# Kernel optimization log

Measured on AMD Instinct MI355X. Metric: run time of the kernel, lower is better.

Reference implementation:

```python
import jax, jax.numpy as jnp
import numpy as np

NEG_SLOPE = 0.2
EPS = 1e-16


def gat_conv(x, edge_index, W, att_src, att_dst, bias, heads, out_ch, concat):
    """PyG-style GATConv (eval mode, add_self_loops=True)."""
    N = x.shape[0]
    h = (x @ W).reshape(N, heads, out_ch)              # [N,H,C]
    loop = jnp.arange(N, dtype=edge_index.dtype)
    src = jnp.concatenate([edge_index[0], loop])       # [E+N]
    dst = jnp.concatenate([edge_index[1], loop])
    a_src = jnp.sum(h * att_src, axis=-1)              # [N,H]
    a_dst = jnp.sum(h * att_dst, axis=-1)
    e = jax.nn.leaky_relu(a_src[src] + a_dst[dst], NEG_SLOPE)  # [E+N,H]
    # segment softmax over destination nodes
    m = jax.ops.segment_max(e, dst, num_segments=N)
    e = jnp.exp(e - m[dst])
    s = jax.ops.segment_sum(e, dst, num_segments=N)
    alpha = e / (s[dst] + EPS)                         # [E+N,H]
    msg = h[src] * alpha[..., None]                    # [E+N,H,C]
    out = jax.ops.segment_sum(msg, dst, num_segments=N)  # [N,H,C]
    out = out.reshape(N, heads * out_ch) if concat else out.mean(axis=1)
    return out + bias


def setup_inputs() -> dict:
    key = jax.random.key(0)
    ks = jax.random.split(key, 11)
    N, F, E = 100000, 128, 1600000
    H1, C1 = 4, 16
    H2, C2 = 1, 16
    return {
        "x": jax.random.normal(ks[0], (N, F), dtype=jnp.float32),
        "edge_index": jax.random.randint(ks[1], (2, E), 0, N, dtype=jnp.int64) if jax.config.jax_enable_x64 else jax.random.randint(ks[1], (2, E), 0, N).astype(jnp.int32),
        "W1": jax.random.normal(ks[2], (F, H1 * C1), dtype=jnp.float32) * 0.1,
        "att_src1": jax.random.normal(ks[3], (H1, C1), dtype=jnp.float32) * 0.1,
        "att_dst1": jax.random.normal(ks[4], (H1, C1), dtype=jnp.float32) * 0.1,
        "bias1": jax.random.normal(ks[5], (H1 * C1,), dtype=jnp.float32) * 0.1,
        "W2": jax.random.normal(ks[6], (H1 * C1, H2 * C2), dtype=jnp.float32) * 0.1,
        "att_src2": jax.random.normal(ks[7], (H2, C2), dtype=jnp.float32) * 0.1,
        "att_dst2": jax.random.normal(ks[8], (H2, C2), dtype=jnp.float32) * 0.1,
        "bias2": jax.random.normal(ks[9], (C2,), dtype=jnp.float32) * 0.1,
    }


def reference(x, edge_index, W1, att_src1, att_dst1, bias1, W2, att_src2, att_dst2, bias2):
    # dropout is identity in eval mode
    h = gat_conv(x, edge_index, W1, att_src1, att_dst1, bias1, heads=4, out_ch=16, concat=True)
    h = jax.nn.elu(h)
    h = gat_conv(h, edge_index, W2, att_src2, att_dst2, bias2, heads=1, out_ch=16, concat=False)
    return jax.nn.log_softmax(h, axis=1)
```

## Files before the change

### kernel.cpp

```cpp
#include <hip/hip_runtime.h>
#include <hip/hip_fp16.h>
#include <hip/hip_bf16.h>
#include <math.h>


#define LRELU(v) ((v) > 0.f ? (v) : 0.2f * (v))
#define BSH 8
#define BCAP 5120
#define CHK 8192

typedef __attribute__((ext_vector_type(8))) short short8;
typedef __attribute__((ext_vector_type(8))) _Float16 half8;
typedef __attribute__((ext_vector_type(4))) _Float16 half4;
typedef __attribute__((ext_vector_type(4))) float float4v;

static __device__ __forceinline__ short f2bf(float f) {
    __hip_bfloat16 b = __float2bfloat16(f);
    return *reinterpret_cast<short*>(&b);
}

__global__ __launch_bounds__(256) void k_scatter(const int* __restrict__ ei, int* __restrict__ cursor,
                                                 int* __restrict__ stage, int E, int NBK) {
    __shared__ int hist[512];
    __shared__ int cnt2[512];
    __shared__ int base[512];
    int tid = threadIdx.x;
    int e0 = blockIdx.x * CHK;
    int nedge = E - e0; if (nedge > CHK) nedge = CHK;

    for (int i = tid; i < 512; i += 256) { hist[i] = 0; cnt2[i] = 0; }
    __syncthreads();
    for (int j = tid; j < nedge; j += 256) {
        int d = ei[E + e0 + j];
        atomicAdd(&hist[d >> BSH], 1);
    }
    __syncthreads();
    for (int b = tid; b < NBK; b += 256) {
        int c = hist[b];
        if (c > 0) base[b] = b * BCAP + atomicAdd(&cursor[b], c);
    }
    __syncthreads();
    for (int j = tid; j < nedge; j += 256) {
        int s = ei[e0 + j];
        int d = ei[E + e0 + j];
        int b = d >> BSH;
        int r = atomicAdd(&cnt2[b], 1);
        stage[base[b] + r] = s | ((d & ((1 << BSH) - 1)) << 17);
    }
}

__global__ __launch_bounds__(256) void k_build(const int* __restrict__ stage,
                                               const int* __restrict__ cursor,
                                               int* __restrict__ row_start,
                                               int* __restrict__ csr,
                                               const float* __restrict__ W1,
                                               const float* __restrict__ att_src,
                                               const float* __restrict__ att_dst,
                                               float* __restrict__ Wc,
                                               const float* __restrict__ W2,
                                               const float* __restrict__ att_src2,
                                               const float* __restrict__ att_dst2,
                                               float* __restrict__ Wc2,
                                               int NBK, int E, int N) {
    __shared__ int cnt[256];
    __shared__ int lb[256];
    __shared__ int cur[256];
    __shared__ int sA[256];
    int b = blockIdx.x, tid = threadIdx.x;
    int nodes0 = b << BSH;
    int nnodes = N - nodes0; if (nnodes > 256) nnodes = 256;
    int partial = 0;
    for (int i = tid; i < b; i += 256) partial += cursor[i];
    sA[tid] = partial;
    __syncthreads();
    for (int off = 128; off >= 1; off >>= 1) {
        if (tid < off) sA[tid] += sA[tid + off];
        __syncthreads();
    }
    int ebase = sA[0];
    int ecnt = cursor[b];
    __syncthreads();
    if (b == 0) {
        if (tid == 0) row_start[N] = E + N;
        for (int i = tid; i < 16 * 128; i += 256) {
            int col = i >> 7, k = i & 127;
            float v = 0.f;
            if (col < 8) {
                int h = col & 3;
                const float* att = (col < 4) ? att_src : att_dst;
                #pragma unroll
                for (int c = 0; c < 16; c++) v += W1[k * 64 + h * 16 + c] * att[h * 16 + c];
            }
            Wc[i] = v;
        }
        for (int i = tid; i < 128; i += 256) {
            int col = i >> 6, k = i & 63;
            const float* att = col ? att_dst2 : att_src2;
            float v = 0.f;
            #pragma unroll
            for (int c = 0; c < 16; c++) v += W2[k * 16 + c] * att[c];
            Wc2[i] = v;
        }
    }
    const int* sbk = stage + b * BCAP;
    cnt[tid] = (tid < nnodes) ? 1 : 0;
    __syncthreads();
    for (int e = tid; e < ecnt; e += 256) {
        int l = (sbk[e] >> 17) & 255;
        atomicAdd(&cnt[l], 1);
    }
    __syncthreads();
    int myc = cnt[tid];
    sA[tid] = myc;
    __syncthreads();
    for (int off = 1; off < 256; off <<= 1) {
        int r = sA[tid] + ((tid >= off) ? sA[tid - off] : 0);
        __syncthreads();
        sA[tid] = r;
        __syncthreads();
    }
    int gb = ebase + nodes0;
    lb[tid] = sA[tid] - myc;
    cur[tid] = 1;
    __syncthreads();
    if (tid < nnodes) {
        row_start[nodes0 + tid] = gb + lb[tid];
        csr[gb + lb[tid]] = nodes0 + tid;
    }
    __syncthreads();
    for (int e = tid; e < ecnt; e += 256) {
        int v = sbk[e];
        int l = (v >> 17) & 255;
        int src = v & 0x1FFFF;
        int r = atomicAdd(&cur[l], 1);
        csr[gb + lb[l] + r] = src;
    }
}

__global__ __launch_bounds__(256) void k_gemm1(const float* __restrict__ x,
                                               const float* __restrict__ W1,
                                               const float* __restrict__ Wc,
                                               __half* __restrict__ h1, float* __restrict__ a_src,
                                               float* __restrict__ a_dst, int N) {
    __shared__ short wt[80 * 136];
    int tid = threadIdx.x;
    for (int i = tid; i < 128 * 64; i += 256) {
        int k = i >> 6, c = i & 63;
        wt[c * 136 + k] = f2bf(W1[i]);
    }
    for (int i = tid; i < 16 * 128; i += 256) {
        int col = i >> 7, k = i & 127;
        wt[(64 + col) * 136 + k] = f2bf(Wc[i]);
    }
    __syncthreads();
    int wave = tid >> 6, lane = tid & 63;
    int m = lane & 15, q = lane >> 4;
    int nbase = blockIdx.x * 64 + wave * 16;
    int anode = nbase + m;
    bool rowok = anode < N;
    const float* xrow = x + (size_t)(rowok ? anode : 0) * 128 + q * 8;

    float4v acc[5];
    #pragma unroll
    for (int ct = 0; ct < 5; ct++)
        #pragma unroll
        for (int r = 0; r < 4; r++) acc[ct][r] = 0.f;

    #pragma unroll
    for (int kc = 0; kc < 4; kc++) {
        float4 u0 = make_float4(0.f, 0.f, 0.f, 0.f), u1 = u0;
        if (rowok) {
            u0 = *(const float4*)(xrow + kc * 32);
            u1 = *(const float4*)(xrow + kc * 32 + 4);
        }
        short8 af;
        af[0] = f2bf(u0.x); af[1] = f2bf(u0.y); af[2] = f2bf(u0.z); af[3] = f2bf(u0.w);
        af[4] = f2bf(u1.x); af[5] = f2bf(u1.y); af[6] = f2bf(u1.z); af[7] = f2bf(u1.w);
        #pragma unroll
        for (int ct = 0; ct < 5; ct++) {
            short8 bf = *(const short8*)&wt[(ct * 16 + m) * 136 + kc * 32 + q * 8];
            acc[ct] = __builtin_amdgcn_mfma_f32_16x16x32_bf16(af, bf, acc[ct], 0, 0, 0);
        }
    }
    #pragma unroll
    for (int ct = 0; ct < 4; ct++) {
        #pragma unroll
        for (int r = 0; r < 4; r++) {
            int n = nbase + q * 4 + r;
            if (n < N) h1[(size_t)n * 64 + ct * 16 + m] = __float2half(acc[ct][r]);
        }
    }
    #pragma unroll
    for (int r = 0; r < 4; r++) {
        int n = nbase + q * 4 + r;
        if (n < N) {
            float v = acc[4][r];
            if (m < 4) a_src[n * 4 + m] = v;
            else if (m < 8) a_dst[n * 4 + (m - 4)] = v;
        }
    }
}

__global__ __launch_bounds__(256) void k_agg1(const int* __restrict__ row_start,
                                              const int* __restrict__ csr_src,
                                              const float* __restrict__ a_src,
                                              const float* __restrict__ a_dst,
                                              const __half* __restrict__ h1,
                                              const float* __restrict__ bias,
                                              __half* __restrict__ out1, int N) {
    int tid = threadIdx.x;
    int wave = tid >> 6, lane = tid & 63;
    int grp = lane >> 2, sub = lane & 3;
    int node = blockIdx.x * 64 + wave * 16 + grp;
    if (node >= N) return;
    int row = row_start[node];
    int deg = row_start[node + 1] - row;
    float adm = a_dst[node * 4 + sub];
    const _Float16* hb = (const _Float16*)h1 + sub * 16;
    float A[16];
    #pragma unroll
    for (int c = 0; c < 16; c++) A[c] = 0.f;
    float sh = 0.f;
    int j = 0;
    for (; j + 4 <= deg; j += 4) {
        int s0 = csr_src[row + j + 0];
        int s1 = csr_src[row + j + 1];
        int s2 = csr_src[row + j + 2];
        int s3 = csr_src[row + j + 3];
        float x0 = a_src[s0 * 4 + sub] + adm;
        float x1 = a_src[s1 * 4 + sub] + adm;
        float x2 = a_src[s2 * 4 + sub] + adm;
        float x3 = a_src[s3 * 4 + sub] + adm;
        half8 p0 = *(const half8*)(hb + (size_t)s0 * 64);
        half8 q0 = *(const half8*)(hb + (size_t)s0 * 64 + 8);
        half8 p1 = *(const half8*)(hb + (size_t)s1 * 64);
        half8 q1 = *(const half8*)(hb + (size_t)s1 * 64 + 8);
        half8 p2 = *(const half8*)(hb + (size_t)s2 * 64);
        half8 q2 = *(const half8*)(hb + (size_t)s2 * 64 + 8);
        half8 p3 = *(const half8*)(hb + (size_t)s3 * 64);
        half8 q3 = *(const half8*)(hb + (size_t)s3 * 64 + 8);
        float e0 = __expf(fmaxf(x0, 0.2f * x0));
        float e1 = __expf(fmaxf(x1, 0.2f * x1));
        float e2 = __expf(fmaxf(x2, 0.2f * x2));
        float e3 = __expf(fmaxf(x3, 0.2f * x3));
        sh += (e0 + e1) + (e2 + e3);
        #pragma unroll
        for (int c = 0; c < 8; c++) {
            A[c]     += e0 * (float)p0[c] + e1 * (float)p1[c]
                      + e2 * (float)p2[c] + e3 * (float)p3[c];
            A[c + 8] += e0 * (float)q0[c] + e1 * (float)q1[c]
                      + e2 * (float)q2[c] + e3 * (float)q3[c];
        }
    }
    for (; j < deg; j++) {
        int s = csr_src[row + j];
        float xv = a_src[s * 4 + sub] + adm;
        half8 p = *(const half8*)(hb + (size_t)s * 64);
        half8 q = *(const half8*)(hb + (size_t)s * 64 + 8);
        float e = __expf(fmaxf(xv, 0.2f * xv));
        sh += e;
        #pragma unroll
        for (int c = 0; c < 8; c++) {
            A[c]     += e * (float)p[c];
            A[c + 8] += e * (float)q[c];
        }
    }
    float iv = 1.f / (sh + 1e-16f);
    const float4* bb = (const float4*)bias + sub * 4;
    union { __half2 h2v[8]; float4 f4[2]; } pk;
    #pragma unroll
    for (int c4 = 0; c4 < 4; c4++) {
        float4 b = bb[c4];
        float o0 = A[c4 * 4 + 0] * iv + b.x;
        float o1 = A[c4 * 4 + 1] * iv + b.y;
        float o2 = A[c4 * 4 + 2] * iv + b.z;
        float o3 = A[c4 * 4 + 3] * iv + b.w;
        o0 = (o0 > 0.f) ? o0 : (__expf(o0) - 1.f);
        o1 = (o1 > 0.f) ? o1 : (__expf(o1) - 1.f);
        o2 = (o2 > 0.f) ? o2 : (__expf(o2) - 1.f);
        o3 = (o3 > 0.f) ? o3 : (__expf(o3) - 1.f);
        pk.h2v[c4 * 2 + 0] = __floats2half2_rn(o0, o1);
        pk.h2v[c4 * 2 + 1] = __floats2half2_rn(o2, o3);
    }
    *(float4*)&out1[(size_t)node * 64 + sub * 16]     = pk.f4[0];
    *(float4*)&out1[(size_t)node * 64 + sub * 16 + 8] = pk.f4[1];
}

__global__ __launch_bounds__(256) void k_gemm2(const __half* __restrict__ out1,
                                               const float* __restrict__ W2,
                                               const float* __restrict__ Wc2,
                                               __half* __restrict__ h2, float* __restrict__ a_src,
                                               float* __restrict__ a_dst, int N) {
    __shared__ _Float16 wt2[16][72];
    __shared__ _Float16 wtb[16][72];
    int tid = threadIdx.x;
    for (int i = tid; i < 16 * 64; i += 256) {
        int k = i >> 4, c = i & 15;
        wt2[c][k] = (_Float16)W2[i];
    }
    for (int i = tid; i < 16 * 64; i += 256) {
        int col = i >> 6, k = i & 63;
        wtb[col][k] = (col < 2) ? (_Float16)Wc2[col * 64 + k] : (_Float16)0.f;
    }
    __syncthreads();
    int wave = tid >> 6, lane = tid & 63;
    int m = lane & 15, q = lane >> 4;
    int nbase = blockIdx.x * 64 + wave * 16;
    int anode = nbase + m;
    bool ok = anode < N;
    const __half* arow = out1 + (size_t)(ok ? anode : 0) * 64 + q * 8;

    float4v c1 = {0.f, 0.f, 0.f, 0.f}, c2v = {0.f, 0.f, 0.f, 0.f};
    #pragma unroll
    for (int kc = 0; kc < 2; kc++) {
        half8 af = *(const half8*)(arow + kc * 32);
        half8 b1 = *(const half8*)&wt2[m][kc * 32 + q * 8];
        half8 b2 = *(const half8*)&wtb[m][kc * 32 + q * 8];
        c1  = __builtin_amdgcn_mfma_f32_16x16x32_f16(af, b1, c1, 0, 0, 0);
        c2v = __builtin_amdgcn_mfma_f32_16x16x32_f16(af, b2, c2v, 0, 0, 0);
    }
    #pragma unroll
    for (int r = 0; r < 4; r++) {
        int n = nbase + q * 4 + r;
        if (n < N) {
            h2[(size_t)n * 16 + m] = __float2half(c1[r]);
            if (m == 0) a_src[n] = c2v[r];
            else if (m == 1) a_dst[n] = c2v[r];
        }
    }
}

__global__ __launch_bounds__(256) void k_agg2(const int* __restrict__ row_start,
                                              const int* __restrict__ csr_src,
                                              const float* __restrict__ a_src,
                                              const float* __restrict__ a_dst,
                                              const __half* __restrict__ h2,
                                              const float* __restrict__ bias,
                                              float* __restrict__ out, int N) {
    int tid = threadIdx.x;
    int wave = tid >> 6, lane = tid & 63;
    int grp = lane >> 2, sub = lane & 3;
    int node = blockIdx.x * 64 + wave * 16 + grp;
    if (node >= N) return;
    int row = row_start[node];
    int deg = row_start[node + 1] - row;
    float ad = a_dst[node];
    const _Float16* hb = (const _Float16*)h2 + sub * 4;
    float A0 = 0.f, A1 = 0.f, A2 = 0.f, A3 = 0.f;
    float sh = 0.f;
    int j = 0;
    for (; j + 4 <= deg; j += 4) {
        int s0 = csr_src[row + j + 0];
        int s1 = csr_src[row + j + 1];
        int s2 = csr_src[row + j + 2];
        int s3 = csr_src[row + j + 3];
        float x0 = a_src[s0] + ad;
        float x1 = a_src[s1] + ad;
        float x2 = a_src[s2] + ad;
        float x3 = a_src[s3] + ad;
        half4 v0 = *(const half4*)(hb + (size_t)s0 * 16);
        half4 v1 = *(const half4*)(hb + (size_t)s1 * 16);
        half4 v2 = *(const half4*)(hb + (size_t)s2 * 16);
        half4 v3 = *(const half4*)(hb + (size_t)s3 * 16);
        float e0 = __expf(fmaxf(x0, 0.2f * x0));
        float e1 = __expf(fmaxf(x1, 0.2f * x1));
        float e2 = __expf(fmaxf(x2, 0.2f * x2));
        float e3 = __expf(fmaxf(x3, 0.2f * x3));
        sh += (e0 + e1) + (e2 + e3);
        A0 += e0 * (float)v0[0] + e1 * (float)v1[0] + e2 * (float)v2[0] + e3 * (float)v3[0];
        A1 += e0 * (float)v0[1] + e1 * (float)v1[1] + e2 * (float)v2[1] + e3 * (float)v3[1];
        A2 += e0 * (float)v0[2] + e1 * (float)v1[2] + e2 * (float)v2[2] + e3 * (float)v3[2];
        A3 += e0 * (float)v0[3] + e1 * (float)v1[3] + e2 * (float)v2[3] + e3 * (float)v3[3];
    }
    for (; j < deg; j++) {
        int s = csr_src[row + j];
        float xv = a_src[s] + ad;
        half4 v = *(const half4*)(hb + (size_t)s * 16);
        float e = __expf(fmaxf(xv, 0.2f * xv));
        sh += e;
        A0 += e * (float)v[0];
        A1 += e * (float)v[1];
        A2 += e * (float)v[2];
        A3 += e * (float)v[3];
    }
    float iv = 1.f / (sh + 1e-16f);
    float4 b = ((const float4*)bias)[sub];
    float v0 = A0 * iv + b.x;
    float v1 = A1 * iv + b.y;
    float v2 = A2 * iv + b.z;
    float v3 = A3 * iv + b.w;
    float mx = fmaxf(fmaxf(v0, v1), fmaxf(v2, v3));
    mx = fmaxf(mx, __shfl_xor(mx, 1, 64));
    mx = fmaxf(mx, __shfl_xor(mx, 2, 64));
    float se = __expf(v0 - mx) + __expf(v1 - mx) + __expf(v2 - mx) + __expf(v3 - mx);
    se += __shfl_xor(se, 1, 64);
    se += __shfl_xor(se, 2, 64);
    float ls = mx + __logf(se);
    *(float4*)&out[(size_t)node * 16 + sub * 4] =
        make_float4(v0 - ls, v1 - ls, v2 - ls, v3 - ls);
}

extern "C" void kernel_launch(void* const* d_in, const int* in_sizes, int n_in,
                              void* d_out, int out_size, void* d_ws, size_t ws_size,
                              hipStream_t stream) {
    const float* x        = (const float*)d_in[0];
    const int*   ei       = (const int*)d_in[1];
    const float* W1       = (const float*)d_in[2];
    const float* att_src1 = (const float*)d_in[3];
    const float* att_dst1 = (const float*)d_in[4];
    const float* bias1    = (const float*)d_in[5];
    const float* W2       = (const float*)d_in[6];
    const float* att_src2 = (const float*)d_in[7];
    const float* att_dst2 = (const float*)d_in[8];
    const float* bias2    = (const float*)d_in[9];
    float* out = (float*)d_out;

    const int N = in_sizes[0] / 128;
    const int E = in_sizes[1] / 2;
    const int NBK = (N + 255) >> BSH;

    char* p = (char*)d_ws;
    auto alloc = [&](size_t bytes) -> void* {
        void* r = (void*)p;
        p += (bytes + 255) & ~(size_t)255;
        return r;
    };
    __half* h1     = (__half*)alloc((size_t)N * 64 * 2);
    __half* out1   = (__half*)alloc((size_t)N * 64 * 2);
    __half* h2     = (__half*)alloc((size_t)N * 16 * 2);
    float* a_src1  = (float*)alloc((size_t)N * 4 * 4);
    float* a_dst1  = (float*)alloc((size_t)N * 4 * 4);
    float* a_src2  = (float*)alloc((size_t)N * 4);
    float* a_dst2  = (float*)alloc((size_t)N * 4);
    float* Wc      = (float*)alloc(16 * 128 * 4);
    float* Wc2     = (float*)alloc(2 * 64 * 4);
    int*   row_st  = (int*)alloc((size_t)(N + 1) * 4);
    int*   csr     = (int*)alloc((size_t)(E + N) * 4);
    int*   stage   = (int*)alloc((size_t)NBK * BCAP * 4);
    int*   cursor  = (int*)alloc((size_t)NBK * 4);
    (void)ws_size; (void)n_in; (void)out_size;

    hipMemsetAsync(cursor, 0, (size_t)NBK * 4, stream);
    k_scatter<<<(E + CHK - 1) / CHK, 256, 0, stream>>>(ei, cursor, stage, E, NBK);
    k_build<<<NBK, 256, 0, stream>>>(stage, cursor, row_st, csr,
                                     W1, att_src1, att_dst1, Wc,
                                     W2, att_src2, att_dst2, Wc2, NBK, E, N);
    k_gemm1<<<(N + 63) / 64, 256, 0, stream>>>(x, W1, Wc, h1, a_src1, a_dst1, N);
    k_agg1<<<(N + 63) / 64, 256, 0, stream>>>(row_st, csr, a_src1, a_dst1, h1, bias1, out1, N);
    k_gemm2<<<(N + 63) / 64, 256, 0, stream>>>(out1, W2, Wc2, h2, a_src2, a_dst2, N);
    k_agg2<<<(N + 63) / 64, 256, 0, stream>>>(row_st, csr, a_src2, a_dst2, h2, bias2, out, N);
}
```

Measured before the change: 236.6 us.

## Split each node's edges across two lane groups and prefetch CSR indices

Both aggregation kernels now give each destination node 8 lanes instead of 4. The two 4-lane halves handle alternating edges, and their partial sums are combined with an xor-shuffle before the epilogue. The next batch of source indices is loaded one iteration ahead so the dependent gathers can issue sooner. This doubles thread-level parallelism on the gather-bound loops, which average about 17 edges per node. The cost is twice as many blocks, extra shuffle reductions, and idle lanes in the epilogue.

```diff
diff --git a/kernel.cpp b/kernel.cpp
--- a/kernel.cpp
+++ b/kernel.cpp
@@ -210,23 +210,23 @@
                                               __half* __restrict__ out1, int N) {
     int tid = threadIdx.x;
     int wave = tid >> 6, lane = tid & 63;
-    int grp = lane >> 2, sub = lane & 3;
-    int node = blockIdx.x * 64 + wave * 16 + grp;
+    int grp = lane >> 3, sub = lane & 3, par = (lane >> 2) & 1;
+    int node = blockIdx.x * 32 + wave * 8 + grp;
     if (node >= N) return;
     int row = row_start[node];
     int deg = row_start[node + 1] - row;
     float adm = a_dst[node * 4 + sub];
     const _Float16* hb = (const _Float16*)h1 + sub * 16;
+    const int* cp = csr_src + row + par;
     float A[16];
     #pragma unroll
     for (int c = 0; c < 16; c++) A[c] = 0.f;
     float sh = 0.f;
+    int c0 = 0, c1 = 0, c2 = 0, c3 = 0;
+    if (deg >= 8) { c0 = cp[0]; c1 = cp[2]; c2 = cp[4]; c3 = cp[6]; }
     int j = 0;
-    for (; j + 4 <= deg; j += 4) {
-        int s0 = csr_src[row + j + 0];
-        int s1 = csr_src[row + j + 1];
-        int s2 = csr_src[row + j + 2];
-        int s3 = csr_src[row + j + 3];
+    for (; j + 8 <= deg; j += 8) {
+        int s0 = c0, s1 = c1, s2 = c2, s3 = c3;
         float x0 = a_src[s0 * 4 + sub] + adm;
         float x1 = a_src[s1 * 4 + sub] + adm;
         float x2 = a_src[s2 * 4 + sub] + adm;
@@ -239,6 +239,9 @@
         half8 q2 = *(const half8*)(hb + (size_t)s2 * 64 + 8);
         half8 p3 = *(const half8*)(hb + (size_t)s3 * 64);
         half8 q3 = *(const half8*)(hb + (size_t)s3 * 64 + 8);
+        if (j + 16 <= deg) {
+            c0 = cp[j + 8]; c1 = cp[j + 10]; c2 = cp[j + 12]; c3 = cp[j + 14];
+        }
         float e0 = __expf(fmaxf(x0, 0.2f * x0));
         float e1 = __expf(fmaxf(x1, 0.2f * x1));
         float e2 = __expf(fmaxf(x2, 0.2f * x2));
@@ -252,38 +255,46 @@
                       + e2 * (float)q2[c] + e3 * (float)q3[c];
         }
     }
-    for (; j < deg; j++) {
-        int s = csr_src[row + j];
-        float xv = a_src[s * 4 + sub] + adm;
-        half8 p = *(const half8*)(hb + (size_t)s * 64);
-        half8 q = *(const half8*)(hb + (size_t)s * 64 + 8);
-        float e = __expf(fmaxf(xv, 0.2f * xv));
-        sh += e;
+    for (; j < deg; j += 2) {
+        int idx = j + par;
+        if (idx < deg) {
+            int s = csr_src[row + idx];
+            float xv = a_src[s * 4 + sub] + adm;
+            half8 p = *(const half8*)(hb + (size_t)s * 64);
+            half8 q = *(const half8*)(hb + (size_t)s * 64 + 8);
+            float e = __expf(fmaxf(xv, 0.2f * xv));
+            sh += e;
+            #pragma unroll
+            for (int c = 0; c < 8; c++) {
+                A[c]     += e * (float)p[c];
+                A[c + 8] += e * (float)q[c];
+            }
+        }
+    }
+    sh += __shfl_xor(sh, 4, 64);
+    #pragma unroll
+    for (int c = 0; c < 16; c++) A[c] += __shfl_xor(A[c], 4, 64);
+    if (par == 0) {
+        float iv = 1.f / (sh + 1e-16f);
+        const float4* bb = (const float4*)bias + sub * 4;
+        union { __half2 h2v[8]; float4 f4[2]; } pk;
         #pragma unroll
-        for (int c = 0; c < 8; c++) {
-            A[c]     += e * (float)p[c];
-            A[c + 8] += e * (float)q[c];
-        }
-    }
-    float iv = 1.f / (sh + 1e-16f);
-    const float4* bb = (const float4*)bias + sub * 4;
-    union { __half2 h2v[8]; float4 f4[2]; } pk;
-    #pragma unroll
-    for (int c4 = 0; c4 < 4; c4++) {
-        float4 b = bb[c4];
-        float o0 = A[c4 * 4 + 0] * iv + b.x;
-        float o1 = A[c4 * 4 + 1] * iv + b.y;
-        float o2 = A[c4 * 4 + 2] * iv + b.z;
-        float o3 = A[c4 * 4 + 3] * iv + b.w;
-        o0 = (o0 > 0.f) ? o0 : (__expf(o0) - 1.f);
-        o1 = (o1 > 0.f) ? o1 : (__expf(o1) - 1.f);
-        o2 = (o2 > 0.f) ? o2 : (__expf(o2) - 1.f);
-        o3 = (o3 > 0.f) ? o3 : (__expf(o3) - 1.f);
-        pk.h2v[c4 * 2 + 0] = __floats2half2_rn(o0, o1);
-        pk.h2v[c4 * 2 + 1] = __floats2half2_rn(o2, o3);
-    }
-    *(float4*)&out1[(size_t)node * 64 + sub * 16]     = pk.f4[0];
-    *(float4*)&out1[(size_t)node * 64 + sub * 16 + 8] = pk.f4[1];
+        for (int c4 = 0; c4 < 4; c4++) {
+            float4 b = bb[c4];
+            float o0 = A[c4 * 4 + 0] * iv + b.x;
+            float o1 = A[c4 * 4 + 1] * iv + b.y;
+            float o2 = A[c4 * 4 + 2] * iv + b.z;
+            float o3 = A[c4 * 4 + 3] * iv + b.w;
+            o0 = (o0 > 0.f) ? o0 : (__expf(o0) - 1.f);
+            o1 = (o1 > 0.f) ? o1 : (__expf(o1) - 1.f);
+            o2 = (o2 > 0.f) ? o2 : (__expf(o2) - 1.f);
+            o3 = (o3 > 0.f) ? o3 : (__expf(o3) - 1.f);
+            pk.h2v[c4 * 2 + 0] = __floats2half2_rn(o0, o1);
+            pk.h2v[c4 * 2 + 1] = __floats2half2_rn(o2, o3);
+        }
+        *(float4*)&out1[(size_t)node * 64 + sub * 16]     = pk.f4[0];
+        *(float4*)&out1[(size_t)node * 64 + sub * 16 + 8] = pk.f4[1];
+    }
 }
 
 __global__ __launch_bounds__(256) void k_gemm2(const __half* __restrict__ out1,
@@ -339,21 +350,21 @@
                                               float* __restrict__ out, int N) {
     int tid = threadIdx.x;
     int wave = tid >> 6, lane = tid & 63;
-    int grp = lane >> 2, sub = lane & 3;
-    int node = blockIdx.x * 64 + wave * 16 + grp;
+    int grp = lane >> 3, sub = lane & 3, par = (lane >> 2) & 1;
+    int node = blockIdx.x * 32 + wave * 8 + grp;
     if (node >= N) return;
     int row = row_start[node];
     int deg = row_start[node + 1] - row;
     float ad = a_dst[node];
     const _Float16* hb = (const _Float16*)h2 + sub * 4;
+    const int* cp = csr_src + row + par;
     float A0 = 0.f, A1 = 0.f, A2 = 0.f, A3 = 0.f;
     float sh = 0.f;
+    int c0 = 0, c1 = 0, c2 = 0, c3 = 0;
+    if (deg >= 8) { c0 = cp[0]; c1 = cp[2]; c2 = cp[4]; c3 = cp[6]; }
     int j = 0;
-    for (; j + 4 <= deg; j += 4) {
-        int s0 = csr_src[row + j + 0];
-        int s1 = csr_src[row + j + 1];
-        int s2 = csr_src[row + j + 2];
-        int s3 = csr_src[row + j + 3];
+    for (; j + 8 <= deg; j += 8) {
+        int s0 = c0, s1 = c1, s2 = c2, s3 = c3;
         float x0 = a_src[s0] + ad;
         float x1 = a_src[s1] + ad;
         float x2 = a_src[s2] + ad;
@@ -362,6 +373,9 @@
         half4 v1 = *(const half4*)(hb + (size_t)s1 * 16);
         half4 v2 = *(const half4*)(hb + (size_t)s2 * 16);
         half4 v3 = *(const half4*)(hb + (size_t)s3 * 16);
+        if (j + 16 <= deg) {
+            c0 = cp[j + 8]; c1 = cp[j + 10]; c2 = cp[j + 12]; c3 = cp[j + 14];
+        }
         float e0 = __expf(fmaxf(x0, 0.2f * x0));
         float e1 = __expf(fmaxf(x1, 0.2f * x1));
         float e2 = __expf(fmaxf(x2, 0.2f * x2));
@@ -372,17 +386,25 @@
         A2 += e0 * (float)v0[2] + e1 * (float)v1[2] + e2 * (float)v2[2] + e3 * (float)v3[2];
         A3 += e0 * (float)v0[3] + e1 * (float)v1[3] + e2 * (float)v2[3] + e3 * (float)v3[3];
     }
-    for (; j < deg; j++) {
-        int s = csr_src[row + j];
-        float xv = a_src[s] + ad;
-        half4 v = *(const half4*)(hb + (size_t)s * 16);
-        float e = __expf(fmaxf(xv, 0.2f * xv));
-        sh += e;
-        A0 += e * (float)v[0];
-        A1 += e * (float)v[1];
-        A2 += e * (float)v[2];
-        A3 += e * (float)v[3];
-    }
+    for (; j < deg; j += 2) {
+        int idx = j + par;
+        if (idx < deg) {
+            int s = csr_src[row + idx];
+            float xv = a_src[s] + ad;
+            half4 v = *(const half4*)(hb + (size_t)s * 16);
+            float e = __expf(fmaxf(xv, 0.2f * xv));
+            sh += e;
+            A0 += e * (float)v[0];
+            A1 += e * (float)v[1];
+            A2 += e * (float)v[2];
+            A3 += e * (float)v[3];
+        }
+    }
+    sh += __shfl_xor(sh, 4, 64);
+    A0 += __shfl_xor(A0, 4, 64);
+    A1 += __shfl_xor(A1, 4, 64);
+    A2 += __shfl_xor(A2, 4, 64);
+    A3 += __shfl_xor(A3, 4, 64);
     float iv = 1.f / (sh + 1e-16f);
     float4 b = ((const float4*)bias)[sub];
     float v0 = A0 * iv + b.x;
@@ -396,8 +418,9 @@
     se += __shfl_xor(se, 1, 64);
     se += __shfl_xor(se, 2, 64);
     float ls = mx + __logf(se);
-    *(float4*)&out[(size_t)node * 16 + sub * 4] =
-        make_float4(v0 - ls, v1 - ls, v2 - ls, v3 - ls);
+    if (par == 0)
+        *(float4*)&out[(size_t)node * 16 + sub * 4] =
+            make_float4(v0 - ls, v1 - ls, v2 - ls, v3 - ls);
 }
 
 extern "C" void kernel_launch(void* const* d_in, const int* in_sizes, int n_in,
@@ -446,7 +469,7 @@
                                      W1, att_src1, att_dst1, Wc,
                                      W2, att_src2, att_dst2, Wc2, NBK, E, N);
     k_gemm1<<<(N + 63) / 64, 256, 0, stream>>>(x, W1, Wc, h1, a_src1, a_dst1, N);
-    k_agg1<<<(N + 63) / 64, 256, 0, stream>>>(row_st, csr, a_src1, a_dst1, h1, bias1, out1, N);
+    k_agg1<<<(N + 31) / 32, 256, 0, stream>>>(row_st, csr, a_src1, a_dst1, h1, bias1, out1, N);
     k_gemm2<<<(N + 63) / 64, 256, 0, stream>>>(out1, W2, Wc2, h2, a_src2, a_dst2, N);
-    k_agg2<<<(N + 63) / 64, 256, 0, stream>>>(row_st, csr, a_src2, a_dst2, h2, bias2, out, N);
-}
+    k_agg2<<<(N + 31) / 32, 256, 0, stream>>>(row_st, csr, a_src2, a_dst2, h2, bias2, out, N);
+}
```

New measurement: 229.4 us. 1.03x faster.
